# Optimization experiments

Measured on AMD Instinct MI355X. Metric: run time of the kernel, lower is better.

## Reference

```python
import jax, jax.numpy as jnp
import numpy as np

N = 50000
E_RAND = 800000
IN_DIM, HIDDEN, OUT_DIM, HEADS = 256, 32, 40, 4


def glorot(key, fan_in, fan_out, shape):
    r = np.sqrt(6.0 / (fan_in + fan_out))
    return jax.random.uniform(key, shape, jnp.float32, -r, r)


def setup_inputs() -> dict:
    key = jax.random.key(0)
    ks = jax.random.split(key, 10)
    x = jax.random.normal(ks[0], (N, IN_DIM), jnp.float32)
    # random edges with src != dst, then append self loops (remove+add_self_loops semantics)
    s = jax.random.randint(ks[1], (E_RAND,), 0, N, jnp.int32)
    d = (s + 1 + jax.random.randint(ks[2], (E_RAND,), 0, N - 1, jnp.int32)) % N
    loops = jnp.arange(N, dtype=jnp.int32)
    src = jnp.concatenate([s, loops])
    dst = jnp.concatenate([d, loops])
    lin1 = glorot(ks[3], IN_DIM, HEADS * HIDDEN, (IN_DIM, HEADS * HIDDEN))
    att_q1 = glorot(ks[4], HEADS, HIDDEN, (1, HEADS, HIDDEN))
    att_v1 = glorot(ks[5], HEADS, HIDDEN, (1, HEADS, HIDDEN))
    bias1 = jnp.zeros((HEADS * HIDDEN,), jnp.float32)
    lin2 = glorot(ks[6], HEADS * HIDDEN, HEADS * OUT_DIM, (HEADS * HIDDEN, HEADS * OUT_DIM))
    att_q2 = glorot(ks[7], HEADS, OUT_DIM, (1, HEADS, OUT_DIM))
    att_v2 = glorot(ks[8], HEADS, OUT_DIM, (1, HEADS, OUT_DIM))
    bias2 = jnp.zeros((OUT_DIM,), jnp.float32)
    return {"x": x, "src": src, "dst": dst,
            "lin1": lin1, "att_q1": att_q1, "att_v1": att_v1, "bias1": bias1,
            "lin2": lin2, "att_q2": att_q2, "att_v2": att_v2, "bias2": bias2}


def segment_softmax(e, seg, n):
    # e: [E, H]; softmax grouped by target node seg
    m = jax.ops.segment_max(e, seg, num_segments=n)  # [N, H]
    ex = jnp.exp(e - m[seg])
    s = jax.ops.segment_sum(ex, seg, num_segments=n)
    return ex / (s[seg] + 1e-16)


def ood_gat_conv(x, src, dst, lin, att_q, att_v, bias, concat):
    n = x.shape[0]
    H, C = att_q.shape[1], att_q.shape[2]
    xh = (x @ lin).reshape(n, H, C)                     # [N, H, C]
    alpha = jnp.sum(xh * att_q, axis=-1)                # [N, H]
    sa = jax.nn.sigmoid(alpha)
    w_alpha = 1.0 - jnp.abs(sa[dst] - sa[src])          # [E, H]
    w_beta = jnp.sum(att_v * jax.nn.leaky_relu(xh[dst] + xh[src]), axis=-1)  # [E, H]
    w = segment_softmax(w_alpha * w_beta, dst, n)       # [E, H]
    out = jax.ops.segment_sum(xh[src] * w[..., None], dst, num_segments=n)  # [N, H, C]
    out = out.reshape(n, H * C) if concat else out.mean(axis=1)
    return out + bias


def reference(x, src, dst, lin1, att_q1, att_v1, bias1, lin2, att_q2, att_v2, bias2):
    h = ood_gat_conv(x, src, dst, lin1, att_q1, att_v1, bias1, concat=True)
    h = jax.nn.elu(h)
    out = ood_gat_conv(h, src, dst, lin2, att_q2, att_v2, bias2, concat=False)
    return out
```

## Files before the change

### kernel.cpp

```cpp
#include <hip/hip_runtime.h>
#include <hip/hip_fp16.h>

#define HEADS 4

typedef _Float16 v2h __attribute__((ext_vector_type(2)));

__device__ __forceinline__ float4 ldh4(const __half* p) {
    const uint2 u = *(const uint2*)p;
    const float2 a = __half22float2(*(const __half2*)&u.x);
    const float2 b = __half22float2(*(const __half2*)&u.y);
    return make_float4(a.x, a.y, b.x, b.y);
}

__device__ __forceinline__ __half2 habs2_(__half2 x) {
    unsigned u = *reinterpret_cast<unsigned*>(&x) & 0x7FFF7FFFu;
    return *reinterpret_cast<__half2*>(&u);
}

__device__ __forceinline__ float fdot2_(__half2 a, __half2 b, float c) {
    return __builtin_amdgcn_fdot2(*(v2h*)&a, *(v2h*)&b, c, false);
}

template <int BN, bool AHALF>
__global__ __launch_bounds__(256)
void gemm_wide_k(const void* __restrict__ Av, const float* __restrict__ B,
                 __half* __restrict__ Cout, int M, int K) {
    constexpr int BM = 128, BK = 32;
    constexpr int MN = BN / 16;
    __shared__ v2h As2[BK / 2][BM];
    __shared__ v2h Bs2[BK / 2][BN];
    const int m0 = blockIdx.x * BM;
    const int tid = threadIdx.x;
    const int ty = tid >> 4;
    const int tx = tid & 15;
    float acc[8][MN] = {};

    for (int kt = 0; kt < K; kt += BK) {
        if (!AHALF) {
            const float* A = (const float*)Av;
            #pragma unroll
            for (int it = 0; it < 4; ++it) {
                const int i = tid + 256 * it;
                const int row = i >> 3;
                const int kc = (i & 7) * 4;
                const int grow = m0 + row;
                float4 v = make_float4(0.f, 0.f, 0.f, 0.f);
                if (grow < M) v = *(const float4*)&A[(size_t)grow * K + kt + kc];
                v2h p0; p0[0] = (_Float16)v.x; p0[1] = (_Float16)v.y;
                v2h p1; p1[0] = (_Float16)v.z; p1[1] = (_Float16)v.w;
                As2[(kc >> 1) + 0][row] = p0;
                As2[(kc >> 1) + 1][row] = p1;
            }
        } else {
            const __half* A = (const __half*)Av;
            #pragma unroll
            for (int it = 0; it < 4; ++it) {
                const int i = tid + 256 * it;
                const int row = i >> 3;
                const int kc = (i & 7) * 4;
                const int grow = m0 + row;
                uint2 u = make_uint2(0u, 0u);
                if (grow < M) u = *(const uint2*)&A[(size_t)grow * K + kt + kc];
                As2[(kc >> 1) + 0][row] = *(v2h*)&u.x;
                As2[(kc >> 1) + 1][row] = *(v2h*)&u.y;
            }
        }
        {
            constexpr int BCH = (BK / 2) * (BN / 4);
            for (int i = tid; i < BCH; i += 256) {
                const int k2 = i / (BN / 4);
                const int n4 = (i % (BN / 4)) * 4;
                const float4 fa = *(const float4*)&B[(size_t)(kt + 2 * k2) * BN + n4];
                const float4 fb = *(const float4*)&B[(size_t)(kt + 2 * k2 + 1) * BN + n4];
                v2h q0; q0[0] = (_Float16)fa.x; q0[1] = (_Float16)fb.x;
                v2h q1; q1[0] = (_Float16)fa.y; q1[1] = (_Float16)fb.y;
                v2h q2; q2[0] = (_Float16)fa.z; q2[1] = (_Float16)fb.z;
                v2h q3; q3[0] = (_Float16)fa.w; q3[1] = (_Float16)fb.w;
                Bs2[k2][n4 + 0] = q0;
                Bs2[k2][n4 + 1] = q1;
                Bs2[k2][n4 + 2] = q2;
                Bs2[k2][n4 + 3] = q3;
            }
        }
        __syncthreads();
        #pragma unroll
        for (int k2 = 0; k2 < BK / 2; ++k2) {
            v2h a_[8], b_[MN];
            #pragma unroll
            for (int i = 0; i < 8; ++i) a_[i] = As2[k2][ty * 8 + i];
            #pragma unroll
            for (int j = 0; j < MN; ++j) b_[j] = Bs2[k2][tx * MN + j];
            #pragma unroll
            for (int i = 0; i < 8; ++i)
                #pragma unroll
                for (int j = 0; j < MN; ++j)
                    acc[i][j] = __builtin_amdgcn_fdot2(a_[i], b_[j], acc[i][j], false);
        }
        __syncthreads();
    }
    #pragma unroll
    for (int i = 0; i < 8; ++i) {
        const int grow = m0 + ty * 8 + i;
        if (grow < M) {
            #pragma unroll
            for (int j = 0; j < MN; j += 2) {
                const __half2 h = __floats2half2_rn(acc[i][j], acc[i][j + 1]);
                *(__half2*)&Cout[(size_t)grow * BN + tx * MN + j] = h;
            }
        }
    }
}

__global__ __launch_bounds__(256)
void alpha_k(const __half* __restrict__ xh, const float* __restrict__ attq,
             float* __restrict__ sa, int n, int C, int HC) {
    const int t = blockIdx.x * blockDim.x + threadIdx.x;
    if (t >= n * HEADS) return;
    const int nd = t >> 2, h = t & 3;
    const __half* xr = &xh[(size_t)nd * HC + h * C];
    const float* q = &attq[h * C];
    float s = 0.f;
    for (int c = 0; c < C; c += 4) {
        float4 a = ldh4(&xr[c]);
        float4 b = *(const float4*)&q[c];
        s += a.x * b.x + a.y * b.y + a.z * b.z + a.w * b.w;
    }
    sa[t] = 1.0f / (1.0f + __expf(-s));
}

__global__ __launch_bounds__(256)
void hist_k(const int* __restrict__ dst, int* __restrict__ deg, int E) {
    int e = blockIdx.x * 256 + threadIdx.x;
    if (e < E) atomicAdd(&deg[dst[e]], 1);
}

__global__ __launch_bounds__(256)
void scan1_k(const int* __restrict__ deg, int* __restrict__ ro,
             int* __restrict__ bsum, int n) {
    __shared__ int s[256];
    int i = blockIdx.x * 256 + threadIdx.x;
    int v = (i < n) ? deg[i] : 0;
    s[threadIdx.x] = v;
    __syncthreads();
    for (int off = 1; off < 256; off <<= 1) {
        int t = (threadIdx.x >= off) ? s[threadIdx.x - off] : 0;
        __syncthreads();
        s[threadIdx.x] += t;
        __syncthreads();
    }
    if (i < n) ro[i] = s[threadIdx.x] - v;
    if (threadIdx.x == 255) bsum[blockIdx.x] = s[255];
}

__global__ __launch_bounds__(256)
void scan2_k(int* __restrict__ bsum, int nb) {
    __shared__ int s[256];
    int v = (threadIdx.x < nb) ? bsum[threadIdx.x] : 0;
    s[threadIdx.x] = v;
    __syncthreads();
    for (int off = 1; off < 256; off <<= 1) {
        int t = (threadIdx.x >= off) ? s[threadIdx.x - off] : 0;
        __syncthreads();
        s[threadIdx.x] += t;
        __syncthreads();
    }
    if (threadIdx.x < nb) bsum[threadIdx.x] = s[threadIdx.x] - v;
}

__global__ __launch_bounds__(256)
void scan3_k(int* __restrict__ ro, int* __restrict__ cur,
             const int* __restrict__ bsum, int n, int E) {
    int i = blockIdx.x * 256 + threadIdx.x;
    if (i < n) {
        int r = ro[i] + bsum[i >> 8];
        ro[i] = r;
        cur[i] = r;
    }
    if (i == 0) ro[n] = E;
}

__global__ __launch_bounds__(256)
void scatter_idx_k(const int* __restrict__ src, const int* __restrict__ dst,
                   int* __restrict__ cur, int* __restrict__ csr_src, int E) {
    int e = blockIdx.x * 256 + threadIdx.x;
    if (e >= E) return;
    int d = dst[e];
    int pos = atomicAdd(&cur[d], 1);
    csr_src[pos] = src[e];
}

template <int C, bool CONCAT>
__global__ __launch_bounds__(256)
void fused_edge_k(const int* __restrict__ ro, const int* __restrict__ csr_src,
                  const __half* __restrict__ xh, const float* __restrict__ sa,
                  const float* __restrict__ attv, const float* __restrict__ bias,
                  void* __restrict__ outp, int n) {
    constexpr int HC = 4 * C;
    constexpr int QH = C / 4;
    constexpr int CHUNK = 64;
    constexpr bool DUAL = (C <= 32);
    const int wid = threadIdx.x >> 6;
    const int lane = threadIdx.x & 63;
    const int node = blockIdx.x * 4 + wid;

    __shared__ float wbuf[4][CHUNK * 4];
    __shared__ int sibuf[4][CHUNK];
    __shared__ __half2 avs[HC / 2];
    for (int i = threadIdx.x; i < HC / 2; i += 256)
        avs[i] = __floats2half2_rn(attv[2 * i], attv[2 * i + 1]);
    __syncthreads();
    if (node >= n) return;

    const int s0 = ro[node], s1 = ro[node + 1];

    const int e_loc = lane >> 2;
    const int h_l = lane & 3;
    const float sad = sa[node * 4 + h_l];
    const __half2 c505 = __floats2half2_rn(0.505f, 0.505f);
    const __half2 c495 = __floats2half2_rn(0.495f, 0.495f);

    __half2 xd[QH * 2];
    {
        const __half* p = &xh[(size_t)node * HC + h_l * C];
        #pragma unroll
        for (int i = 0; i < QH; ++i) {
            const uint2 u = *(const uint2*)&p[i * 4];
            xd[2 * i] = *(const __half2*)&u.x;
            xd[2 * i + 1] = *(const __half2*)&u.y;
        }
    }

    const int half_ = DUAL ? (lane >> 5) : 0;
    const int q = DUAL ? (lane & 31) : lane;
    const int h_a = (q < C) ? (q / QH) : 0;

    float4 acc = make_float4(0.f, 0.f, 0.f, 0.f);
    float ssum = 0.f;

    for (int base = s0; base < s1; base += CHUNK) {
        const int cnt = min(CHUNK, s1 - base);
        const int npass = (cnt + 15) >> 4;
        for (int p = 0; p < npass; ++p) {
            const int eidx = p * 16 + e_loc;
            const int j = base + eidx;
            float w = 0.f;
            int si = 0;
            if (j < s1) {
                si = csr_src[j];
                const float sas = sa[si * 4 + h_l];
                const float wa = 1.0f - fabsf(sad - sas);
                const __half* xs = &xh[(size_t)si * HC + h_l * C];
                float wb = 0.f;
                #pragma unroll
                for (int i = 0; i < QH; ++i) {
                    const uint2 u = *(const uint2*)&xs[i * 4];
                    const __half2 a0 = *(const __half2*)&u.x;
                    const __half2 a1 = *(const __half2*)&u.y;
                    const __half2 t0 = __hadd2(a0, xd[2 * i]);
                    const __half2 t1 = __hadd2(a1, xd[2 * i + 1]);
                    const __half2 l0 = __hfma2(t0, c505, __hmul2(habs2_(t0), c495));
                    const __half2 l1 = __hfma2(t1, c505, __hmul2(habs2_(t1), c495));
                    wb = fdot2_(l0, avs[h_l * QH * 2 + 2 * i], wb);
                    wb = fdot2_(l1, avs[h_l * QH * 2 + 2 * i + 1], wb);
                }
                w = __expf(fminf(wa * wb, 60.f));
                ssum += w;
            }
            wbuf[wid][eidx * 4 + h_l] = w;
            if (h_l == 0) sibuf[wid][eidx] = si;
        }
        const int padded = npass << 4;
        if (q < C) {
            if (DUAL) {
                for (int i = 0; i < padded; i += 8) {
                    const int e0 = i + half_, e1 = i + half_ + 2;
                    const int e2 = i + half_ + 4, e3 = i + half_ + 6;
                    const int i0 = sibuf[wid][e0], i1 = sibuf[wid][e1];
                    const int i2 = sibuf[wid][e2], i3 = sibuf[wid][e3];
                    const float w0 = wbuf[wid][e0 * 4 + h_a];
                    const float w1 = wbuf[wid][e1 * 4 + h_a];
                    const float w2 = wbuf[wid][e2 * 4 + h_a];
                    const float w3 = wbuf[wid][e3 * 4 + h_a];
                    const float4 v0 = ldh4(&xh[(size_t)i0 * HC + q * 4]);
                    const float4 v1 = ldh4(&xh[(size_t)i1 * HC + q * 4]);
                    const float4 v2 = ldh4(&xh[(size_t)i2 * HC + q * 4]);
                    const float4 v3 = ldh4(&xh[(size_t)i3 * HC + q * 4]);
                    acc.x += w0 * v0.x + w1 * v1.x + w2 * v2.x + w3 * v3.x;
                    acc.y += w0 * v0.y + w1 * v1.y + w2 * v2.y + w3 * v3.y;
                    acc.z += w0 * v0.z + w1 * v1.z + w2 * v2.z + w3 * v3.z;
                    acc.w += w0 * v0.w + w1 * v1.w + w2 * v2.w + w3 * v3.w;
                }
            } else {
                for (int i = 0; i < padded; i += 4) {
                    const int i0 = sibuf[wid][i],     i1 = sibuf[wid][i + 1];
                    const int i2 = sibuf[wid][i + 2], i3 = sibuf[wid][i + 3];
                    const float w0 = wbuf[wid][(i + 0) * 4 + h_a];
                    const float w1 = wbuf[wid][(i + 1) * 4 + h_a];
                    const float w2 = wbuf[wid][(i + 2) * 4 + h_a];
                    const float w3 = wbuf[wid][(i + 3) * 4 + h_a];
                    const float4 v0 = ldh4(&xh[(size_t)i0 * HC + q * 4]);
                    const float4 v1 = ldh4(&xh[(size_t)i1 * HC + q * 4]);
                    const float4 v2 = ldh4(&xh[(size_t)i2 * HC + q * 4]);
                    const float4 v3 = ldh4(&xh[(size_t)i3 * HC + q * 4]);
                    acc.x += w0 * v0.x + w1 * v1.x + w2 * v2.x + w3 * v3.x;
                    acc.y += w0 * v0.y + w1 * v1.y + w2 * v2.y + w3 * v3.y;
                    acc.z += w0 * v0.z + w1 * v1.z + w2 * v2.z + w3 * v3.z;
                    acc.w += w0 * v0.w + w1 * v1.w + w2 * v2.w + w3 * v3.w;
                }
            }
        }
    }

    if (DUAL) {
        acc.x += __shfl_xor(acc.x, 32, 64);
        acc.y += __shfl_xor(acc.y, 32, 64);
        acc.z += __shfl_xor(acc.z, 32, 64);
        acc.w += __shfl_xor(acc.w, 32, 64);
    }

    #pragma unroll
    for (int off = 4; off < 64; off <<= 1) ssum += __shfl_xor(ssum, off, 64);
    const float stot = __shfl(ssum, h_a, 64);
    const float inv = 1.0f / (stot + 1e-20f);
    acc.x *= inv; acc.y *= inv; acc.z *= inv; acc.w *= inv;

    if (CONCAT) {
        if (q < C && half_ == 0) {
            const float4 b = ((const float4*)bias)[q];
            float4 v = make_float4(acc.x + b.x, acc.y + b.y, acc.z + b.z, acc.w + b.w);
            v.x = v.x > 0.f ? v.x : __expf(v.x) - 1.0f;
            v.y = v.y > 0.f ? v.y : __expf(v.y) - 1.0f;
            v.z = v.z > 0.f ? v.z : __expf(v.z) - 1.0f;
            v.w = v.w > 0.f ? v.w : __expf(v.w) - 1.0f;
            __half* o16 = (__half*)outp;
            const __half2 h01 = __floats2half2_rn(v.x, v.y);
            const __half2 h23 = __floats2half2_rn(v.z, v.w);
            uint2 u;
            u.x = *(const unsigned*)&h01;
            u.y = *(const unsigned*)&h23;
            *(uint2*)&o16[(size_t)node * HC + q * 4] = u;
        }
    } else {
        const int qq = (q < QH) ? q : 0;
        const float x1 = __shfl(acc.x, qq + QH, 64);
        const float y1 = __shfl(acc.y, qq + QH, 64);
        const float z1 = __shfl(acc.z, qq + QH, 64);
        const float w1 = __shfl(acc.w, qq + QH, 64);
        const float x2 = __shfl(acc.x, qq + 2 * QH, 64);
        const float y2 = __shfl(acc.y, qq + 2 * QH, 64);
        const float z2 = __shfl(acc.z, qq + 2 * QH, 64);
        const float w2 = __shfl(acc.w, qq + 2 * QH, 64);
        const float x3 = __shfl(acc.x, qq + 3 * QH, 64);
        const float y3 = __shfl(acc.y, qq + 3 * QH, 64);
        const float z3 = __shfl(acc.z, qq + 3 * QH, 64);
        const float w3 = __shfl(acc.w, qq + 3 * QH, 64);
        if (q < QH && half_ == 0) {
            float* of = (float*)outp;
            const float4 b = ((const float4*)bias)[q];
            float4 v;
            v.x = 0.25f * (acc.x + x1 + x2 + x3) + b.x;
            v.y = 0.25f * (acc.y + y1 + y2 + y3) + b.y;
            v.z = 0.25f * (acc.z + z1 + z2 + z3) + b.z;
            v.w = 0.25f * (acc.w + w1 + w2 + w3) + b.w;
            *(float4*)&of[(size_t)node * C + q * 4] = v;
        }
    }
}

extern "C" void kernel_launch(void* const* d_in, const int* in_sizes, int n_in,
                              void* d_out, int out_size, void* d_ws, size_t ws_size,
                              hipStream_t stream) {
    const float* x      = (const float*)d_in[0];
    const int*   src    = (const int*)d_in[1];
    const int*   dst    = (const int*)d_in[2];
    const float* lin1   = (const float*)d_in[3];
    const float* att_q1 = (const float*)d_in[4];
    const float* att_v1 = (const float*)d_in[5];
    const float* bias1  = (const float*)d_in[6];
    const float* lin2   = (const float*)d_in[7];
    const float* att_q2 = (const float*)d_in[8];
    const float* att_v2 = (const float*)d_in[9];
    const float* bias2  = (const float*)d_in[10];
    float* outp = (float*)d_out;

    const int n = in_sizes[0] / 256;
    const int E = in_sizes[1];
    const int nh = n * HEADS;
    const int NB = (n + 255) / 256;

    char* wsb = (char*)d_ws;
    size_t o = 0;
    __half* xh    = (__half*)(wsb + o); o += (size_t)n * 160 * 2;
    __half* acc16 = (__half*)(wsb + o); o += (size_t)n * 128 * 2;
    float* sa     = (float*)(wsb + o); o += (size_t)nh * 4;
    int* csr_src  = (int*)(wsb + o); o += (size_t)E * 4;
    int* deg      = (int*)(wsb + o); o += (size_t)n * 4;
    int* ro       = (int*)(wsb + o); o += (size_t)(n + 1) * 4;
    int* cur      = (int*)(wsb + o); o += (size_t)n * 4;
    int* bsum     = (int*)(wsb + o); o += 256 * 4;

    dim3 blk(256);
    const int EG = (E + 255) / 256;
    const int MB = (n + 127) / 128;

    hipMemsetAsync(deg, 0, (size_t)n * 4, stream);
    hist_k<<<EG, blk, 0, stream>>>(dst, deg, E);
    scan1_k<<<NB, blk, 0, stream>>>(deg, ro, bsum, n);
    scan2_k<<<1, blk, 0, stream>>>(bsum, NB);
    scan3_k<<<NB, blk, 0, stream>>>(ro, cur, bsum, n, E);
    scatter_idx_k<<<EG, blk, 0, stream>>>(src, dst, cur, csr_src, E);

    gemm_wide_k<128, false><<<MB, blk, 0, stream>>>(x, lin1, xh, n, 256);
    alpha_k<<<(nh + 255) / 256, blk, 0, stream>>>(xh, att_q1, sa, n, 32, 128);
    fused_edge_k<32, true><<<(n + 3) / 4, blk, 0, stream>>>(ro, csr_src, xh, sa, att_v1, bias1, acc16, n);

    gemm_wide_k<160, true><<<MB, blk, 0, stream>>>(acc16, lin2, xh, n, 128);
    alpha_k<<<(nh + 255) / 256, blk, 0, stream>>>(xh, att_q2, sa, n, 40, 160);
    fused_edge_k<40, false><<<(n + 3) / 4, blk, 0, stream>>>(ro, csr_src, xh, sa, att_v2, bias2, outp, n);
}
```

Baseline: 355.7 us.

## Fuse attention-alpha into GEMM epilogue and merge histogram into first GEMM launch

The per-node sigmoid(alpha) computation moves into the GEMM epilogue, using a shared-memory atomic reduction per row and head, so the separate alpha kernels and their re-read of xh go away. The degree histogram now runs as extra blocks of the first GEMM launch, which removes a launch and lets the histogram overlap the GEMM. The GEMM tile is halved from 128 to 64 rows, giving more blocks but less reuse per block. The alpha dot product now uses the fp32 accumulators instead of the rounded fp16 outputs, which slightly changes numerics.

After: 331.9 us. -6.7%, faster.

```diff
diff --git a/kernel.cpp b/kernel.cpp
--- a/kernel.cpp
+++ b/kernel.cpp
@@ -22,24 +22,30 @@
 }
 
 template <int BN, bool AHALF>
-__global__ __launch_bounds__(256)
-void gemm_wide_k(const void* __restrict__ Av, const float* __restrict__ B,
-                 __half* __restrict__ Cout, int M, int K) {
-    constexpr int BM = 128, BK = 32;
+__device__ __forceinline__ void gemm_alpha_body(
+    const void* __restrict__ Av, const float* __restrict__ B,
+    const float* __restrict__ attq, __half* __restrict__ Cout,
+    float* __restrict__ sa, int M, int K, int bid) {
+    constexpr int BM = 64, BK = 32;
     constexpr int MN = BN / 16;
+    constexpr int C = BN / 4;
     __shared__ v2h As2[BK / 2][BM];
     __shared__ v2h Bs2[BK / 2][BN];
-    const int m0 = blockIdx.x * BM;
+    __shared__ float sred[BM][4];
+    __shared__ float aq[BN];
+    const int m0 = bid * BM;
     const int tid = threadIdx.x;
     const int ty = tid >> 4;
     const int tx = tid & 15;
-    float acc[8][MN] = {};
+    for (int i = tid; i < BN; i += 256) aq[i] = attq[i];
+    sred[tid >> 2][tid & 3] = 0.f;
+    float acc[4][MN] = {};
 
     for (int kt = 0; kt < K; kt += BK) {
         if (!AHALF) {
             const float* A = (const float*)Av;
             #pragma unroll
-            for (int it = 0; it < 4; ++it) {
+            for (int it = 0; it < 2; ++it) {
                 const int i = tid + 256 * it;
                 const int row = i >> 3;
                 const int kc = (i & 7) * 4;
@@ -54,7 +60,7 @@
         } else {
             const __half* A = (const __half*)Av;
             #pragma unroll
-            for (int it = 0; it < 4; ++it) {
+            for (int it = 0; it < 2; ++it) {
                 const int i = tid + 256 * it;
                 const int row = i >> 3;
                 const int kc = (i & 7) * 4;
@@ -85,53 +91,63 @@
         __syncthreads();
         #pragma unroll
         for (int k2 = 0; k2 < BK / 2; ++k2) {
-            v2h a_[8], b_[MN];
-            #pragma unroll
-            for (int i = 0; i < 8; ++i) a_[i] = As2[k2][ty * 8 + i];
+            v2h a_[4], b_[MN];
+            #pragma unroll
+            for (int i = 0; i < 4; ++i) a_[i] = As2[k2][ty * 4 + i];
             #pragma unroll
             for (int j = 0; j < MN; ++j) b_[j] = Bs2[k2][tx * MN + j];
             #pragma unroll
-            for (int i = 0; i < 8; ++i)
+            for (int i = 0; i < 4; ++i)
                 #pragma unroll
                 for (int j = 0; j < MN; ++j)
                     acc[i][j] = __builtin_amdgcn_fdot2(a_[i], b_[j], acc[i][j], false);
         }
         __syncthreads();
     }
+    const int cbase = tx * MN;
+    const int head = cbase / C;
     #pragma unroll
-    for (int i = 0; i < 8; ++i) {
-        const int grow = m0 + ty * 8 + i;
+    for (int i = 0; i < 4; ++i) {
+        const int grow = m0 + ty * 4 + i;
         if (grow < M) {
             #pragma unroll
             for (int j = 0; j < MN; j += 2) {
                 const __half2 h = __floats2half2_rn(acc[i][j], acc[i][j + 1]);
-                *(__half2*)&Cout[(size_t)grow * BN + tx * MN + j] = h;
-            }
-        }
-    }
-}
-
-__global__ __launch_bounds__(256)
-void alpha_k(const __half* __restrict__ xh, const float* __restrict__ attq,
-             float* __restrict__ sa, int n, int C, int HC) {
-    const int t = blockIdx.x * blockDim.x + threadIdx.x;
-    if (t >= n * HEADS) return;
-    const int nd = t >> 2, h = t & 3;
-    const __half* xr = &xh[(size_t)nd * HC + h * C];
-    const float* q = &attq[h * C];
-    float s = 0.f;
-    for (int c = 0; c < C; c += 4) {
-        float4 a = ldh4(&xr[c]);
-        float4 b = *(const float4*)&q[c];
-        s += a.x * b.x + a.y * b.y + a.z * b.z + a.w * b.w;
-    }
-    sa[t] = 1.0f / (1.0f + __expf(-s));
-}
-
-__global__ __launch_bounds__(256)
-void hist_k(const int* __restrict__ dst, int* __restrict__ deg, int E) {
-    int e = blockIdx.x * 256 + threadIdx.x;
-    if (e < E) atomicAdd(&deg[dst[e]], 1);
+                *(__half2*)&Cout[(size_t)grow * BN + cbase + j] = h;
+            }
+            float part = 0.f;
+            #pragma unroll
+            for (int j = 0; j < MN; ++j) part += acc[i][j] * aq[cbase + j];
+            atomicAdd(&sred[ty * 4 + i][head], part);
+        }
+    }
+    __syncthreads();
+    {
+        const int row = m0 + (tid >> 2);
+        if (row < M)
+            sa[row * 4 + (tid & 3)] =
+                1.0f / (1.0f + __expf(-sred[tid >> 2][tid & 3]));
+    }
+}
+
+__global__ __launch_bounds__(256)
+void front_k(const float* __restrict__ x, const float* __restrict__ lin1,
+             const float* __restrict__ attq1, __half* __restrict__ xh,
+             float* __restrict__ sa, const int* __restrict__ dst,
+             int* __restrict__ deg, int M, int K, int MB, int E) {
+    if ((int)blockIdx.x < MB) {
+        gemm_alpha_body<128, false>(x, lin1, attq1, xh, sa, M, K, blockIdx.x);
+    } else {
+        const int e = (blockIdx.x - MB) * 256 + threadIdx.x;
+        if (e < E) atomicAdd(&deg[dst[e]], 1);
+    }
+}
+
+__global__ __launch_bounds__(256)
+void gemm2_k(const __half* __restrict__ acc16, const float* __restrict__ lin2,
+             const float* __restrict__ attq2, __half* __restrict__ xh,
+             float* __restrict__ sa, int M, int K) {
+    gemm_alpha_body<160, true>(acc16, lin2, attq2, xh, sa, M, K, blockIdx.x);
 }
 
 __global__ __launch_bounds__(256)
@@ -401,20 +417,18 @@
 
     dim3 blk(256);
     const int EG = (E + 255) / 256;
-    const int MB = (n + 127) / 128;
+    const int MB = (n + 63) / 64;
 
     hipMemsetAsync(deg, 0, (size_t)n * 4, stream);
-    hist_k<<<EG, blk, 0, stream>>>(dst, deg, E);
+    front_k<<<MB + EG, blk, 0, stream>>>(x, lin1, att_q1, xh, sa, dst, deg,
+                                         n, 256, MB, E);
     scan1_k<<<NB, blk, 0, stream>>>(deg, ro, bsum, n);
     scan2_k<<<1, blk, 0, stream>>>(bsum, NB);
     scan3_k<<<NB, blk, 0, stream>>>(ro, cur, bsum, n, E);
     scatter_idx_k<<<EG, blk, 0, stream>>>(src, dst, cur, csr_src, E);
 
-    gemm_wide_k<128, false><<<MB, blk, 0, stream>>>(x, lin1, xh, n, 256);
-    alpha_k<<<(nh + 255) / 256, blk, 0, stream>>>(xh, att_q1, sa, n, 32, 128);
     fused_edge_k<32, true><<<(n + 3) / 4, blk, 0, stream>>>(ro, csr_src, xh, sa, att_v1, bias1, acc16, n);
 
-    gemm_wide_k<160, true><<<MB, blk, 0, stream>>>(acc16, lin2, xh, n, 128);
-    alpha_k<<<(nh + 255) / 256, blk, 0, stream>>>(xh, att_q2, sa, n, 40, 160);
+    gemm2_k<<<MB, blk, 0, stream>>>(acc16, lin2, att_q2, xh, sa, n, 128);
     fused_edge_k<40, false><<<(n + 3) / 4, blk, 0, stream>>>(ro, csr_src, xh, sa, att_v2, bias2, outp, n);
 }
```
